# Performance work log

Hardware: AMD Instinct MI355X
Metric: run time of the kernel (lower is better)

Reference implementation:

```python
import jax, jax.numpy as jnp
import numpy as np
import itertools

N_ELEC = 128
BOX_L = 10.0
DIM = 3
BATCH = 4096


def gen_kpoints(N, L, dim):
    # Faithful numpy port of genKpoints (FermiNet make_kpoints variant).
    rec = 2.0 * np.pi / L
    dk = 1.0 + 1e-05
    max_k = int((N * dk) ** (1.0 / dim) + 0.5)
    ordinals = sorted(range(-max_k, max_k + 1), key=abs)
    ords = np.array(list(itertools.product(ordinals, repeat=dim)), dtype=np.float64)
    kpoints = ords * rec
    order = np.argsort(np.linalg.norm(kpoints, axis=1), kind='stable')
    kpoints = kpoints[order]
    return kpoints[:N].astype(np.float32)


def make_switches(kpoints, dim):
    # Select cos for k-points on the 'positive' side, sin(-k.r) for the rest.
    weights = 10.0 ** np.arange(1, dim + 1)
    weighted_sums = np.sign(kpoints).dot(weights)
    k_signs = np.sign(weighted_sums + 1.0)
    cos_switch = ((k_signs + 1.0) / 2.0).astype(np.float32)
    sin_switch = ((1.0 - k_signs) / 2.0).astype(np.float32)
    return cos_switch, sin_switch


def setup_inputs() -> dict:
    key = jax.random.key(0)
    rs = jax.random.uniform(key, (BATCH, N_ELEC, DIM), dtype=jnp.float32) * BOX_L
    kpoints = gen_kpoints(N_ELEC, BOX_L, DIM)
    cos_switch, sin_switch = make_switches(kpoints, DIM)
    return {
        'rs': rs,
        'kpoints': jnp.asarray(kpoints),
        'cos_switch': jnp.asarray(cos_switch),
        'sin_switch': jnp.asarray(sin_switch),
    }


def reference(rs, kpoints, cos_switch, sin_switch):
    # dots[b, i, m] = k_m . r_{b,i}   -> [B, N, N]
    dots = jnp.einsum('bnd,md->bnm', rs, kpoints)
    # Slater matrix: rows = particles, cols = plane-wave orbitals.
    slater = cos_switch * jnp.cos(dots) + sin_switch * jnp.sin(-dots)
    # log |det| per walker (batched LU) -> [B]
    return jnp.linalg.slogdet(slater)[1]
```

## Files before the change

kernel.cpp:

```cpp
#include <hip/hip_runtime.h>
#include <stdint.h>

#define NM 128
#define NT 1024

typedef float v2f __attribute__((ext_vector_type(2)));

__device__ __forceinline__ float readlane_f(float v, int lane) {
    return __int_as_float(__builtin_amdgcn_readlane(__float_as_int(v), lane));
}

__device__ __forceinline__ unsigned wave_max_dpp(unsigned x) {
    int v = (int)x;
#define DPP_STEP(ctrl) \
    { int o = __builtin_amdgcn_update_dpp(0, v, ctrl, 0xf, 0xf, true); \
      v = ((unsigned)o > (unsigned)v) ? o : v; }
    DPP_STEP(0x111)
    DPP_STEP(0x112)
    DPP_STEP(0x114)
    DPP_STEP(0x118)
    DPP_STEP(0x142)
    DPP_STEP(0x143)
#undef DPP_STEP
    return (unsigned)v;
}

__device__ __forceinline__ unsigned pack_key(float v, int r) {
    return (((__float_as_uint(v) & 0x7fffffffu) >> 6) << 7) | (unsigned)r;
}

__device__ __forceinline__ unsigned argmax_bcast(unsigned ka, unsigned kb) {
    const unsigned m = wave_max_dpp(ka > kb ? ka : kb);
    return (unsigned)__builtin_amdgcn_readlane((int)m, 63);
}

__device__ __forceinline__ float sel_readlane(v2f c, int p) {
    return (p < 64) ? readlane_f(c.x, p) : readlane_f(c.y, p - 64);
}

template<int B>
__device__ __forceinline__ void factor8(v2f (&sv)[16], bool& elim0, bool& elim1,
                                        int r0, int r1, int l, int g,
                                        float2 (*colvg)[64],
                                        unsigned* keysM, float* pivsM,
                                        ulonglong2* masksM) {
    const bool e0in = elim0, e1in = elim1;
    __builtin_amdgcn_s_setprio(1);
#pragma unroll
    for (int i = 0; i < 8; ++i) {
        const v2f c = sv[B + i];
        const unsigned key = argmax_bcast(elim0 ? 0u : pack_key(c.x, r0),
                                          elim1 ? 0u : pack_key(c.y, r1));
        const int pu = __builtin_amdgcn_readfirstlane((int)(key & 127u));
        const float piv = sel_readlane(c, pu);
        const float rcp = __builtin_amdgcn_rcpf(piv);
        elim0 = elim0 || (r0 == pu);
        elim1 = elim1 || (r1 == pu);
        const v2f lm = { elim0 ? 0.0f : c.x * rcp,
                         elim1 ? 0.0f : c.y * rcp };
        colvg[i][l] = make_float2(lm.x, lm.y);
        float u[8];
        if (pu < 64) {
#pragma unroll
            for (int m = i + 1; m < 8; ++m) u[m] = readlane_f(sv[B + m].x, pu);
        } else {
#pragma unroll
            for (int m = i + 1; m < 8; ++m) u[m] = readlane_f(sv[B + m].y, pu - 64);
        }
#pragma unroll
        for (int m = i + 1; m < 8; ++m)
            sv[B + m] = __builtin_elementwise_fma((v2f){-u[m], -u[m]}, lm, sv[B + m]);
        if (l == 0) { keysM[8 * g + i] = key; pivsM[8 * g + i] = piv; }
    }
    __builtin_amdgcn_s_setprio(0);
    const unsigned long long b0 = __ballot(elim0 && !e0in);
    const unsigned long long b1 = __ballot(elim1 && !e1in);
    if (l == 0) masksM[g] = make_ulonglong2(b0, b1);
}

__device__ __forceinline__ void decode_p(const unsigned* keysR, int (&p)[8]) {
    const uint4 ka = *(const uint4*)&keysR[0];
    const uint4 kb = *(const uint4*)&keysR[4];
    p[0] = __builtin_amdgcn_readfirstlane((int)(ka.x & 127u));
    p[1] = __builtin_amdgcn_readfirstlane((int)(ka.y & 127u));
    p[2] = __builtin_amdgcn_readfirstlane((int)(ka.z & 127u));
    p[3] = __builtin_amdgcn_readfirstlane((int)(ka.w & 127u));
    p[4] = __builtin_amdgcn_readfirstlane((int)(kb.x & 127u));
    p[5] = __builtin_amdgcn_readfirstlane((int)(kb.y & 127u));
    p[6] = __builtin_amdgcn_readfirstlane((int)(kb.z & 127u));
    p[7] = __builtin_amdgcn_readfirstlane((int)(kb.w & 127u));
}

template<int B>
__device__ __forceinline__ void apply8(v2f (&sv)[16], const int (&p)[8],
                                       const float2 (*cp)[64], int l) {
#pragma unroll
    for (int i = 0; i < 8; ++i) {
        const float2 la = cp[i][l];
        const v2f lm = (v2f){la.x, la.y};
        float u[8];
        if (p[i] < 64) {
#pragma unroll
            for (int j = 0; j < 8; ++j) u[j] = readlane_f(sv[B + j].x, p[i]);
        } else {
#pragma unroll
            for (int j = 0; j < 8; ++j) u[j] = readlane_f(sv[B + j].y, p[i] - 64);
        }
#pragma unroll
        for (int j = 0; j < 8; ++j)
            sv[B + j] = __builtin_elementwise_fma((v2f){-u[j], -u[j]}, lm, sv[B + j]);
    }
}

__global__ __launch_bounds__(NT, 8)
void slater_logdet(const float* __restrict__ rs,
                   const float* __restrict__ kpts,
                   const float* __restrict__ csw,
                   const float* __restrict__ ssw,
                   float* __restrict__ out) {
    __shared__ float2 colv[2][2][8][64];
    __shared__ unsigned keysF[2][NM];
    __shared__ float    pivsF[2][NM];
    __shared__ ulonglong2 masks[2][16];
    __shared__ float    redf[4];

    const int t  = threadIdx.x;
    const int bA = 2 * blockIdx.x;
    const int bB = 2 * blockIdx.x + 1;
    const int w  = t >> 6;
    const int l  = t & 63;
    const int r0 = l, r1 = l + 64;

    v2f sv[16];
    {
        const float* rsA = rs + (size_t)bA * NM * 3;
        const float* rsB = rs + (size_t)bB * NM * 3;
        const float ax0 = rsA[r0 * 3 + 0], ay0 = rsA[r0 * 3 + 1], az0 = rsA[r0 * 3 + 2];
        const float ax1 = rsA[r1 * 3 + 0], ay1 = rsA[r1 * 3 + 1], az1 = rsA[r1 * 3 + 2];
        const float bx0 = rsB[r0 * 3 + 0], by0 = rsB[r0 * 3 + 1], bz0 = rsB[r0 * 3 + 2];
        const float bx1 = rsB[r1 * 3 + 0], by1 = rsB[r1 * 3 + 1], bz1 = rsB[r1 * 3 + 2];
#pragma unroll
        for (int j = 0; j < 16; ++j) {
            const int m = (j < 8) ? (8 * w + j) : (8 * (15 - w) + (j - 8));
            const float kx = kpts[m * 3 + 0], ky = kpts[m * 3 + 1], kz = kpts[m * 3 + 2];
            const float cw = csw[m], sw = ssw[m];
            float sn, cn;
            if (j < 8) {
                __sincosf(kx * ax0 + ky * ay0 + kz * az0, &sn, &cn);
                sv[j].x = cw * cn - sw * sn;
                __sincosf(kx * ax1 + ky * ay1 + kz * az1, &sn, &cn);
                sv[j].y = cw * cn - sw * sn;
            } else {
                __sincosf(kx * bx0 + ky * by0 + kz * bz0, &sn, &cn);
                sv[j].x = cw * cn - sw * sn;
                __sincosf(kx * bx1 + ky * by1 + kz * bz1, &sn, &cn);
                sv[j].y = cw * cn - sw * sn;
            }
        }
    }

    bool eA0 = false, eA1 = false, eB0 = false, eB1 = false;

    if (w == 0)
        factor8<0>(sv, eA0, eA1, r0, r1, l, 0, colv[0][0],
                   keysF[0], pivsF[0], masks[0]);
    if (w == 15)
        factor8<8>(sv, eB0, eB1, r0, r1, l, 0, colv[1][0],
                   keysF[1], pivsF[1], masks[1]);
    __syncthreads();

    for (int rd = 0; rd < 15; ++rd) {
        const int par = rd & 1;
        if (rd < w) {
            const ulonglong2 mk = masks[0][rd];
            eA0 = eA0 || (((mk.x >> l) & 1ull) != 0);
            eA1 = eA1 || (((mk.y >> l) & 1ull) != 0);
            int p[8];
            decode_p(&keysF[0][8 * rd], p);
            apply8<0>(sv, p, colv[0][par], l);
            if (rd == w - 1)
                factor8<0>(sv, eA0, eA1, r0, r1, l, rd + 1,
                           colv[0][(rd + 1) & 1], keysF[0], pivsF[0], masks[0]);
        }
        if (rd < 15 - w) {
            const ulonglong2 mk = masks[1][rd];
            eB0 = eB0 || (((mk.x >> l) & 1ull) != 0);
            eB1 = eB1 || (((mk.y >> l) & 1ull) != 0);
            int p[8];
            decode_p(&keysF[1][8 * rd], p);
            apply8<8>(sv, p, colv[1][par], l);
            if (rd == 14 - w)
                factor8<8>(sv, eB0, eB1, r0, r1, l, rd + 1,
                           colv[1][(rd + 1) & 1], keysF[1], pivsF[1], masks[1]);
        }
        __syncthreads();
    }

    float lg = 0.0f;
    if (t < 256) {
        const int mat = t >> 7;
        lg = __logf(fabsf(pivsF[mat][t & 127]));
#pragma unroll
        for (int off = 32; off > 0; off >>= 1)
            lg += __shfl_xor(lg, off, 64);
        if ((t & 63) == 0) redf[t >> 6] = lg;
    }
    __syncthreads();
    if (t == 0) out[bA] = redf[0] + redf[1];
    if (t == 1) out[bB] = redf[2] + redf[3];
}

extern "C" void kernel_launch(void* const* d_in, const int* in_sizes, int n_in,
                              void* d_out, int out_size, void* d_ws, size_t ws_size,
                              hipStream_t stream) {
    const float* rs = (const float*)d_in[0];
    const float* kp = (const float*)d_in[1];
    const float* cs = (const float*)d_in[2];
    const float* ss = (const float*)d_in[3];
    float* out = (float*)d_out;
    const int batch = in_sizes[0] / (NM * 3);
    slater_logdet<<<dim3(batch / 2), dim3(NT), 0, stream>>>(rs, kp, cs, ss, out);
}
```

Before: 388.8 us.

## Halve block to 512 threads with each wave owning 32 columns across two matrices

```diff
diff --git a/kernel.cpp b/kernel.cpp
--- a/kernel.cpp
+++ b/kernel.cpp
@@ -2,7 +2,7 @@
 #include <stdint.h>
 
 #define NM 128
-#define NT 1024
+#define NT 512
 
 typedef float v2f __attribute__((ext_vector_type(2)));
 
@@ -39,11 +39,59 @@
 }
 
 template<int B>
-__device__ __forceinline__ void factor8(v2f (&sv)[16], bool& elim0, bool& elim1,
-                                        int r0, int r1, int l, int g,
-                                        float2 (*colvg)[64],
-                                        unsigned* keysM, float* pivsM,
-                                        ulonglong2* masksM) {
+__device__ __forceinline__ void apply8T(v2f (&sv)[32], int p, v2f lmn) {
+    float u[8];
+    if (p < 64) {
+#pragma unroll
+        for (int j = 0; j < 8; ++j) u[j] = readlane_f(sv[B + j].x, p);
+#pragma unroll
+        for (int j = 0; j < 8; ++j)
+            sv[B + j] = __builtin_elementwise_fma((v2f){u[j], u[j]}, lmn, sv[B + j]);
+    } else {
+        const int q = p - 64;
+#pragma unroll
+        for (int j = 0; j < 8; ++j) u[j] = readlane_f(sv[B + j].y, q);
+#pragma unroll
+        for (int j = 0; j < 8; ++j)
+            sv[B + j] = __builtin_elementwise_fma((v2f){u[j], u[j]}, lmn, sv[B + j]);
+    }
+}
+
+template<int B>
+__device__ __forceinline__ void apply16T(v2f (&sv)[32], int p, v2f lmn) {
+    float u[8];
+    if (p < 64) {
+#pragma unroll
+        for (int j = 0; j < 8; ++j) u[j] = readlane_f(sv[B + j].x, p);
+#pragma unroll
+        for (int j = 0; j < 8; ++j)
+            sv[B + j] = __builtin_elementwise_fma((v2f){u[j], u[j]}, lmn, sv[B + j]);
+#pragma unroll
+        for (int j = 0; j < 8; ++j) u[j] = readlane_f(sv[B + 8 + j].x, p);
+#pragma unroll
+        for (int j = 0; j < 8; ++j)
+            sv[B + 8 + j] = __builtin_elementwise_fma((v2f){u[j], u[j]}, lmn, sv[B + 8 + j]);
+    } else {
+        const int q = p - 64;
+#pragma unroll
+        for (int j = 0; j < 8; ++j) u[j] = readlane_f(sv[B + j].y, q);
+#pragma unroll
+        for (int j = 0; j < 8; ++j)
+            sv[B + j] = __builtin_elementwise_fma((v2f){u[j], u[j]}, lmn, sv[B + j]);
+#pragma unroll
+        for (int j = 0; j < 8; ++j) u[j] = readlane_f(sv[B + 8 + j].y, q);
+#pragma unroll
+        for (int j = 0; j < 8; ++j)
+            sv[B + 8 + j] = __builtin_elementwise_fma((v2f){u[j], u[j]}, lmn, sv[B + 8 + j]);
+    }
+}
+
+template<int B>
+__device__ __forceinline__ void lookahead8(v2f (&sv)[32], bool& elim0, bool& elim1,
+                                           int r0, int r1, int l, int g,
+                                           float2 (*colvg)[64],
+                                           unsigned* keysM, float* pivsM,
+                                           ulonglong2* masksM) {
     const bool e0in = elim0, e1in = elim1;
     __builtin_amdgcn_s_setprio(1);
 #pragma unroll
@@ -53,12 +101,12 @@
                                           elim1 ? 0u : pack_key(c.y, r1));
         const int pu = __builtin_amdgcn_readfirstlane((int)(key & 127u));
         const float piv = sel_readlane(c, pu);
-        const float rcp = __builtin_amdgcn_rcpf(piv);
+        const float rcpn = -__builtin_amdgcn_rcpf(piv);
         elim0 = elim0 || (r0 == pu);
         elim1 = elim1 || (r1 == pu);
-        const v2f lm = { elim0 ? 0.0f : c.x * rcp,
-                         elim1 ? 0.0f : c.y * rcp };
-        colvg[i][l] = make_float2(lm.x, lm.y);
+        const v2f lmn = { elim0 ? 0.0f : c.x * rcpn,
+                          elim1 ? 0.0f : c.y * rcpn };
+        colvg[i][l] = make_float2(lmn.x, lmn.y);
         float u[8];
         if (pu < 64) {
 #pragma unroll
@@ -69,7 +117,7 @@
         }
 #pragma unroll
         for (int m = i + 1; m < 8; ++m)
-            sv[B + m] = __builtin_elementwise_fma((v2f){-u[m], -u[m]}, lm, sv[B + m]);
+            sv[B + m] = __builtin_elementwise_fma((v2f){u[m], u[m]}, lmn, sv[B + m]);
         if (l == 0) { keysM[8 * g + i] = key; pivsM[8 * g + i] = piv; }
     }
     __builtin_amdgcn_s_setprio(0);
@@ -91,28 +139,53 @@
     p[7] = __builtin_amdgcn_readfirstlane((int)(kb.w & 127u));
 }
 
-template<int B>
-__device__ __forceinline__ void apply8(v2f (&sv)[16], const int (&p)[8],
-                                       const float2 (*cp)[64], int l) {
-#pragma unroll
-    for (int i = 0; i < 8; ++i) {
-        const float2 la = cp[i][l];
-        const v2f lm = (v2f){la.x, la.y};
-        float u[8];
-        if (p[i] < 64) {
-#pragma unroll
-            for (int j = 0; j < 8; ++j) u[j] = readlane_f(sv[B + j].x, p[i]);
-        } else {
-#pragma unroll
-            for (int j = 0; j < 8; ++j) u[j] = readlane_f(sv[B + j].y, p[i] - 64);
-        }
-#pragma unroll
-        for (int j = 0; j < 8; ++j)
-            sv[B + j] = __builtin_elementwise_fma((v2f){-u[j], -u[j]}, lm, sv[B + j]);
-    }
-}
-
-__global__ __launch_bounds__(NT, 8)
+template<int BASE>
+__device__ __forceinline__ void matrixRound(v2f (&sv)[32], bool& e0, bool& e1,
+                                            int rd, int wOwn, int r0, int r1, int l,
+                                            float2 (*colvM)[8][64],
+                                            unsigned* keysM, float* pivsM,
+                                            ulonglong2* masksM) {
+    if (rd > wOwn + 7) return;
+    const ulonglong2 mk = masksM[rd];
+    e0 = e0 || (((mk.x >> l) & 1ull) != 0);
+    e1 = e1 || (((mk.y >> l) & 1ull) != 0);
+    int p[8];
+    decode_p(&keysM[8 * rd], p);
+    const float2 (*cp)[64] = colvM[rd & 1];
+    if (rd < wOwn - 1) {
+#pragma unroll
+        for (int i = 0; i < 8; ++i) {
+            const float2 la = cp[i][l];
+            apply16T<BASE>(sv, p[i], (v2f){la.x, la.y});
+        }
+    } else if (rd == wOwn - 1) {
+        __builtin_amdgcn_s_setprio(1);
+#pragma unroll
+        for (int i = 0; i < 8; ++i) {
+            const float2 la = cp[i][l];
+            apply8T<BASE>(sv, p[i], (v2f){la.x, la.y});
+        }
+        lookahead8<BASE>(sv, e0, e1, r0, r1, l, rd + 1,
+                         colvM[(rd + 1) & 1], keysM, pivsM, masksM);
+#pragma unroll
+        for (int i = 0; i < 8; ++i) {
+            const float2 la = cp[i][l];
+            apply8T<BASE + 8>(sv, p[i], (v2f){la.x, la.y});
+        }
+        __builtin_amdgcn_s_setprio(0);
+    } else {
+#pragma unroll
+        for (int i = 0; i < 8; ++i) {
+            const float2 la = cp[i][l];
+            apply8T<BASE + 8>(sv, p[i], (v2f){la.x, la.y});
+        }
+        if (rd == wOwn + 7)
+            lookahead8<BASE + 8>(sv, e0, e1, r0, r1, l, rd + 1,
+                                 colvM[(rd + 1) & 1], keysM, pivsM, masksM);
+    }
+}
+
+__global__ __launch_bounds__(NT, 6)
 void slater_logdet(const float* __restrict__ rs,
                    const float* __restrict__ kpts,
                    const float* __restrict__ csw,
@@ -128,70 +201,56 @@
     const int bA = 2 * blockIdx.x;
     const int bB = 2 * blockIdx.x + 1;
     const int w  = t >> 6;
+    const int w2 = w ^ 1;
     const int l  = t & 63;
     const int r0 = l, r1 = l + 64;
 
-    v2f sv[16];
+    v2f sv[32];
     {
         const float* rsA = rs + (size_t)bA * NM * 3;
+#pragma unroll
+        for (int j = 0; j < 16; ++j) {
+            const int m = (j < 8) ? (8 * w + j) : (64 + 8 * w + (j - 8));
+            const float kx = kpts[m * 3 + 0], ky = kpts[m * 3 + 1], kz = kpts[m * 3 + 2];
+            const float d0 = kx * rsA[r0 * 3] + ky * rsA[r0 * 3 + 1] + kz * rsA[r0 * 3 + 2];
+            const float d1 = kx * rsA[r1 * 3] + ky * rsA[r1 * 3 + 1] + kz * rsA[r1 * 3 + 2];
+            if (csw[m] != 0.0f) { sv[j].x = __cosf(d0);  sv[j].y = __cosf(d1); }
+            else                { sv[j].x = -__sinf(d0); sv[j].y = -__sinf(d1); }
+        }
         const float* rsB = rs + (size_t)bB * NM * 3;
-        const float ax0 = rsA[r0 * 3 + 0], ay0 = rsA[r0 * 3 + 1], az0 = rsA[r0 * 3 + 2];
-        const float ax1 = rsA[r1 * 3 + 0], ay1 = rsA[r1 * 3 + 1], az1 = rsA[r1 * 3 + 2];
-        const float bx0 = rsB[r0 * 3 + 0], by0 = rsB[r0 * 3 + 1], bz0 = rsB[r0 * 3 + 2];
-        const float bx1 = rsB[r1 * 3 + 0], by1 = rsB[r1 * 3 + 1], bz1 = rsB[r1 * 3 + 2];
 #pragma unroll
         for (int j = 0; j < 16; ++j) {
-            const int m = (j < 8) ? (8 * w + j) : (8 * (15 - w) + (j - 8));
+            const int m = (j < 8) ? (8 * w2 + j) : (64 + 8 * w2 + (j - 8));
             const float kx = kpts[m * 3 + 0], ky = kpts[m * 3 + 1], kz = kpts[m * 3 + 2];
-            const float cw = csw[m], sw = ssw[m];
-            float sn, cn;
-            if (j < 8) {
-                __sincosf(kx * ax0 + ky * ay0 + kz * az0, &sn, &cn);
-                sv[j].x = cw * cn - sw * sn;
-                __sincosf(kx * ax1 + ky * ay1 + kz * az1, &sn, &cn);
-                sv[j].y = cw * cn - sw * sn;
-            } else {
-                __sincosf(kx * bx0 + ky * by0 + kz * bz0, &sn, &cn);
-                sv[j].x = cw * cn - sw * sn;
-                __sincosf(kx * bx1 + ky * by1 + kz * bz1, &sn, &cn);
-                sv[j].y = cw * cn - sw * sn;
-            }
+            const float d0 = kx * rsB[r0 * 3] + ky * rsB[r0 * 3 + 1] + kz * rsB[r0 * 3 + 2];
+            const float d1 = kx * rsB[r1 * 3] + ky * rsB[r1 * 3 + 1] + kz * rsB[r1 * 3 + 2];
+            if (csw[m] != 0.0f) { sv[16 + j].x = __cosf(d0);  sv[16 + j].y = __cosf(d1); }
+            else                { sv[16 + j].x = -__sinf(d0); sv[16 + j].y = -__sinf(d1); }
         }
     }
 
     bool eA0 = false, eA1 = false, eB0 = false, eB1 = false;
 
     if (w == 0)
-        factor8<0>(sv, eA0, eA1, r0, r1, l, 0, colv[0][0],
-                   keysF[0], pivsF[0], masks[0]);
-    if (w == 15)
-        factor8<8>(sv, eB0, eB1, r0, r1, l, 0, colv[1][0],
-                   keysF[1], pivsF[1], masks[1]);
+        lookahead8<0>(sv, eA0, eA1, r0, r1, l, 0, colv[0][0],
+                      keysF[0], pivsF[0], masks[0]);
+    if (w2 == 0)
+        lookahead8<16>(sv, eB0, eB1, r0, r1, l, 0, colv[1][0],
+                       keysF[1], pivsF[1], masks[1]);
     __syncthreads();
 
     for (int rd = 0; rd < 15; ++rd) {
-        const int par = rd & 1;
-        if (rd < w) {
-            const ulonglong2 mk = masks[0][rd];
-            eA0 = eA0 || (((mk.x >> l) & 1ull) != 0);
-            eA1 = eA1 || (((mk.y >> l) & 1ull) != 0);
-            int p[8];
-            decode_p(&keysF[0][8 * rd], p);
-            apply8<0>(sv, p, colv[0][par], l);
-            if (rd == w - 1)
-                factor8<0>(sv, eA0, eA1, r0, r1, l, rd + 1,
-                           colv[0][(rd + 1) & 1], keysF[0], pivsF[0], masks[0]);
-        }
-        if (rd < 15 - w) {
-            const ulonglong2 mk = masks[1][rd];
-            eB0 = eB0 || (((mk.x >> l) & 1ull) != 0);
-            eB1 = eB1 || (((mk.y >> l) & 1ull) != 0);
-            int p[8];
-            decode_p(&keysF[1][8 * rd], p);
-            apply8<8>(sv, p, colv[1][par], l);
-            if (rd == 14 - w)
-                factor8<8>(sv, eB0, eB1, r0, r1, l, rd + 1,
-                           colv[1][(rd + 1) & 1], keysF[1], pivsF[1], masks[1]);
+        const bool fac2 = (rd == w2 - 1) || (rd == w2 + 7);
+        if (fac2) {
+            matrixRound<16>(sv, eB0, eB1, rd, w2, r0, r1, l,
+                            colv[1], keysF[1], pivsF[1], masks[1]);
+            matrixRound<0>(sv, eA0, eA1, rd, w, r0, r1, l,
+                           colv[0], keysF[0], pivsF[0], masks[0]);
+        } else {
+            matrixRound<0>(sv, eA0, eA1, rd, w, r0, r1, l,
+                           colv[0], keysF[0], pivsF[0], masks[0]);
+            matrixRound<16>(sv, eB0, eB1, rd, w2, r0, r1, l,
+                            colv[1], keysF[1], pivsF[1], masks[1]);
         }
         __syncthreads();
     }
```

Measured after the change: 456.7 us. +17.5%, slower.
